# Kernel tuning notes

Hardware: AMD Instinct MI355X
Metric: run time of the kernel (lower is better)

## Reference

```python
import jax, jax.numpy as jnp
import numpy as np

N_NODES = 50000
N_EDGES = 400000
N_GRAPHS = 16
IN_DIM_NODE = 6
IN_DIM_EDGE = 2
HIDDEN = 64
N_LAYERS = 3
STATE_DIM = 4
MLP1, MLP2 = 256, 256
MAX_ACTION = 1.0
BN_EPS = 1e-5


def _lin(key, fan_in, fan_out):
    k1, k2 = jax.random.split(key)
    s = 1.0 / np.sqrt(fan_in)
    w = jax.random.uniform(k1, (fan_in, fan_out), minval=-s, maxval=s, dtype=jnp.float32)
    b = jax.random.uniform(k2, (fan_out,), minval=-s, maxval=s, dtype=jnp.float32)
    return w, b


def setup_inputs() -> dict:
    key = jax.random.key(0)
    ks = jax.random.split(key, 32)
    inp = {}
    inp["state"] = jax.random.normal(ks[0], (N_GRAPHS, STATE_DIM), dtype=jnp.float32)
    inp["h_feat"] = jax.random.normal(ks[1], (N_NODES, IN_DIM_NODE), dtype=jnp.float32)
    # positive edge features (distances) bounded away from 0 since forward takes 1/e
    inp["e_feat"] = jax.random.uniform(ks[2], (N_EDGES, IN_DIM_EDGE), minval=0.5, maxval=1.5, dtype=jnp.float32)
    inp["src"] = jax.random.randint(ks[3], (N_EDGES,), 0, N_NODES, dtype=jnp.int32)
    inp["dst"] = jax.random.randint(ks[4], (N_EDGES,), 0, N_NODES, dtype=jnp.int32)
    inp["graph_ids"] = jnp.sort(jax.random.randint(ks[5], (N_NODES,), 0, N_GRAPHS, dtype=jnp.int32))
    inp["emb_h_w"], inp["emb_h_b"] = _lin(ks[6], IN_DIM_NODE, HIDDEN)
    inp["emb_e_w"], inp["emb_e_b"] = _lin(ks[7], IN_DIM_EDGE, HIDDEN)
    for i, name in enumerate(["A", "B", "C", "D", "E"]):
        ws, bs = [], []
        for l in range(N_LAYERS):
            w, b = _lin(jax.random.fold_in(ks[8 + i], l), HIDDEN, HIDDEN)
            ws.append(w); bs.append(b)
        inp[name + "_w"] = jnp.stack(ws)  # [L, H, H]
        inp[name + "_b"] = jnp.stack(bs)  # [L, H]
    inp["bn_h_g"] = jnp.ones((N_LAYERS, HIDDEN), jnp.float32)
    inp["bn_h_b"] = jnp.zeros((N_LAYERS, HIDDEN), jnp.float32)
    inp["bn_e_g"] = jnp.ones((N_LAYERS, HIDDEN), jnp.float32)
    inp["bn_e_b"] = jnp.zeros((N_LAYERS, HIDDEN), jnp.float32)
    inp["l1_w"], inp["l1_b"] = _lin(ks[13], HIDDEN + STATE_DIM, MLP1)
    inp["l2_w"], inp["l2_b"] = _lin(ks[14], MLP1, MLP2)
    inp["l3_w"], inp["l3_b"] = _lin(ks[15], MLP2, 2)
    return inp


def _bn(x, g, b):
    mu = jnp.mean(x, axis=0)
    var = jnp.var(x, axis=0)
    return (x - mu) * jax.lax.rsqrt(var + BN_EPS) * g + b


def reference(state, h_feat, e_feat, src, dst, graph_ids,
              emb_h_w, emb_h_b, emb_e_w, emb_e_b,
              A_w, A_b, B_w, B_b, C_w, C_b, D_w, D_b, E_w, E_b,
              bn_h_g, bn_h_b, bn_e_g, bn_e_b,
              l1_w, l1_b, l2_w, l2_b, l3_w, l3_b):
    N = h_feat.shape[0]
    B = state.shape[0]
    # feature prep: concat node states, reciprocal edge states
    e = 1.0 / e_feat
    h = h_feat @ emb_h_w + emb_h_b          # [N, H]
    e = e @ emb_e_w + emb_e_b               # [E, H]
    for l in range(N_LAYERS):
        h_in, e_in = h, e
        Ah = h @ A_w[l] + A_b[l]
        Bh = h @ B_w[l] + B_b[l]
        Dh = h @ D_w[l] + D_b[l]
        Eh = h @ E_w[l] + E_b[l]
        Ce = e @ C_w[l] + C_b[l]
        e_hat = Dh[src] + Eh[dst] + Ce      # [E, H] edge gates pre-activation
        sigma = jax.nn.sigmoid(e_hat)
        num = jax.ops.segment_sum(sigma * Bh[src], dst, num_segments=N)
        den = jax.ops.segment_sum(sigma, dst, num_segments=N)
        h_new = Ah + num / (den + 1e-6)
        h = h_in + jax.nn.relu(_bn(h_new, bn_h_g[l], bn_h_b[l]))
        e = e_in + jax.nn.relu(_bn(e_hat, bn_e_g[l], bn_e_b[l]))
    # mean readout per graph
    counts = jax.ops.segment_sum(jnp.ones((N,), h.dtype), graph_ids, num_segments=B)
    hg = jax.ops.segment_sum(h, graph_ids, num_segments=B) / counts[:, None]
    x = jnp.concatenate([hg, state], axis=-1)
    x = jax.nn.relu(x @ l1_w + l1_b)
    x = jax.nn.relu(x @ l2_w + l2_b)
    return MAX_ACTION * jnp.tanh(x @ l3_w + l3_b)
```

## Files before the change

kernel.cpp:

```cpp
#include <hip/hip_runtime.h>
#include <hip/hip_fp16.h>
#include <math.h>
#include <string.h>

#define NN 50000
#define NE 400000

__device__ __forceinline__ void atomAddF(float* p, float v) { unsafeAtomicAdd(p, v); }
__device__ __forceinline__ double atomAddD(double* p, double v) { return unsafeAtomicAdd(p, v); }
__device__ __forceinline__ int atomAddI(int* p, int v) { return atomicAdd(p, v); }

typedef _Float16 h2v __attribute__((ext_vector_type(2)));

__device__ __forceinline__ float2 up2h(unsigned v) {
  __half2 h; memcpy(&h, &v, 4); return __half22float2(h);
}
__device__ __forceinline__ unsigned pk2h(float a, float b) {
  __half2 h = __floats2half2_rn(a, b);
  unsigned v; memcpy(&v, &h, 4); return v;
}
__device__ __forceinline__ void up8(uint4 u, float* f) {
  float2 a = up2h(u.x), b = up2h(u.y), c = up2h(u.z), d = up2h(u.w);
  f[0] = a.x; f[1] = a.y; f[2] = b.x; f[3] = b.y;
  f[4] = c.x; f[5] = c.y; f[6] = d.x; f[7] = d.y;
}
__device__ __forceinline__ uint4 pk8(const float* f) {
  uint4 u;
  u.x = pk2h(f[0], f[1]); u.y = pk2h(f[2], f[3]);
  u.z = pk2h(f[4], f[5]); u.w = pk2h(f[6], f[7]);
  return u;
}

#if __has_builtin(__builtin_amdgcn_fdot2)
__device__ __forceinline__ float dot2(unsigned a, unsigned b, float c) {
  return __builtin_amdgcn_fdot2(__builtin_bit_cast(h2v, a), __builtin_bit_cast(h2v, b), c, false);
}
#else
__device__ __forceinline__ float dot2(unsigned a, unsigned b, float c) {
  float2 fa = up2h(a), fb = up2h(b);
  return c + fa.x * fb.x + fa.y * fb.y;
}
#endif

#define SW(kk) ((((kk) & 7)) << 2)

__global__ __launch_bounds__(256) void k_zero(float4* __restrict__ p, int n4) {
  int i = blockIdx.x * 256 + threadIdx.x;
  int s = gridDim.x * 256;
  for (; i < n4; i += s) p[i] = make_float4(0.f, 0.f, 0.f, 0.f);
}

__global__ __launch_bounds__(256) void k_deg(const int* __restrict__ dst, int* __restrict__ deg) {
  int i = blockIdx.x * 256 + threadIdx.x;
  if (i < NE) atomAddI(&deg[dst[i]], 1);
}

__global__ __launch_bounds__(1024) void k_scan(int* __restrict__ degcur,
    int* __restrict__ offs, double* __restrict__ stats) {
  __shared__ int wsum[16];
  int t = threadIdx.x;
  int lane = t & 63, w = t >> 6;
  if (t < 256) stats[t] = 0.0;
  int carry = 0;
  for (int base = 0; base < NN; base += 1024) {
    int i = base + t;
    int v = (i < NN) ? degcur[i] : 0;
    int x = v;
    #pragma unroll
    for (int off = 1; off < 64; off <<= 1) {
      int y = __shfl_up(x, off);
      if (lane >= off) x += y;
    }
    if (lane == 63) wsum[w] = x;
    __syncthreads();
    if (w == 0 && lane < 16) {
      int s = wsum[lane];
      #pragma unroll
      for (int off = 1; off < 16; off <<= 1) {
        int y = __shfl_up(s, off);
        if (lane >= off) s += y;
      }
      wsum[lane] = s;
    }
    __syncthreads();
    int wbase = (w > 0) ? wsum[w - 1] : 0;
    int total = wsum[15];
    int excl = carry + wbase + x - v;
    if (i < NN) { offs[i] = excl; degcur[i] = excl; }
    carry += total;
    __syncthreads();
  }
  if (t == 0) offs[NN] = carry;
}

__global__ __launch_bounds__(256) void k_scatter(const int* __restrict__ dst,
    const int* __restrict__ src, const float* __restrict__ e_feat,
    int* __restrict__ cursor,
    int* __restrict__ srcp, int* __restrict__ dstp, float* __restrict__ ef2) {
  int i = blockIdx.x * 256 + threadIdx.x;
  if (i < NE) {
    int d = dst[i];
    int p = atomAddI(&cursor[d], 1);
    srcp[p] = src[i];
    dstp[p] = d;
    ((float2*)ef2)[p] = ((const float2*)e_feat)[i];
  }
}

template <int MODE>
__global__ __launch_bounds__(512) void k_node_gemm(float* __restrict__ h,
    const float* __restrict__ Ah_in, const float* __restrict__ bnp,
    const float* __restrict__ hf, const float* __restrict__ ehw,
    const float* __restrict__ ehb,
    const float* __restrict__ w0, const float* __restrict__ w1,
    const float* __restrict__ w2, const float* __restrict__ w3,
    const float* __restrict__ b0, const float* __restrict__ b1,
    const float* __restrict__ b2, const float* __restrict__ b3,
    float* __restrict__ Ah, __half* __restrict__ Bh16,
    __half* __restrict__ Dh16, __half* __restrict__ Eh16) {
  __shared__ __align__(16) unsigned hsU[32 * 256];
  __shared__ __align__(16) unsigned wshU[32 * 64];
  int t = threadIdx.x;
  int n0 = blockIdx.x * 256;
  #pragma unroll
  for (int i = 0; i < 8; ++i) {
    int f = (t + i * 512) * 4;
    int r = f >> 6;
    int k = f & 63;
    int n = n0 + r;
    float4 v = make_float4(0.f, 0.f, 0.f, 0.f);
    if (n < NN) {
      size_t idx = (size_t)n * 64 + k;
      if (MODE == 2) {
        const float* row = hf + (size_t)n * 6;
        v = *(const float4*)(ehb + k);
        #pragma unroll
        for (int q = 0; q < 6; ++q) {
          float x = row[q];
          float4 wv = *(const float4*)(ehw + q * 64 + k);
          v.x += x * wv.x; v.y += x * wv.y; v.z += x * wv.z; v.w += x * wv.w;
        }
        *(float4*)(h + idx) = v;
      } else {
        v = *(const float4*)(h + idx);
        if (MODE == 1) {
          float4 av = *(const float4*)(Ah_in + idx);
          float4 sc4 = *(const float4*)(bnp + k);
          float4 sh4 = *(const float4*)(bnp + 64 + k);
          v.x += fmaxf(av.x * sc4.x + sh4.x, 0.f);
          v.y += fmaxf(av.y * sc4.y + sh4.y, 0.f);
          v.z += fmaxf(av.z * sc4.z + sh4.z, 0.f);
          v.w += fmaxf(av.w * sc4.w + sh4.w, 0.f);
          *(float4*)(h + idx) = v;
        }
      }
    }
    int kk0 = k >> 1;
    hsU[(kk0 + 0) * 256 + (r ^ SW(kk0 + 0))] = pk2h(v.x, v.y);
    hsU[(kk0 + 1) * 256 + (r ^ SW(kk0 + 1))] = pk2h(v.z, v.w);
  }
  int cg = t & 7, rg = t >> 3;
  int cb = cg * 8;
  #pragma unroll 1
  for (int y = 0; y < 4; ++y) {
    const float* W = (y == 0) ? w0 : (y == 1) ? w1 : (y == 2) ? w2 : w3;
    const float* B = (y == 0) ? b0 : (y == 1) ? b1 : (y == 2) ? b2 : b3;
    __syncthreads();
    #pragma unroll
    for (int i = 0; i < 4; ++i) {
      int idx = t + i * 512;
      int kk = idx >> 6, j = idx & 63;
      wshU[idx] = pk2h(W[(2 * kk) * 64 + j], W[(2 * kk + 1) * 64 + j]);
    }
    __syncthreads();
    float acc[4][8];
    #pragma unroll
    for (int r = 0; r < 4; ++r)
      #pragma unroll
      for (int j = 0; j < 8; ++j) acc[r][j] = 0.f;
    #pragma unroll 8
    for (int kk = 0; kk < 32; ++kk) {
      uint4 a4 = *(const uint4*)&hsU[kk * 256 + ((rg * 4) ^ SW(kk))];
      uint4 wA = *(const uint4*)&wshU[kk * 64 + cb];
      uint4 wB = *(const uint4*)&wshU[kk * 64 + cb + 4];
      unsigned av[4] = {a4.x, a4.y, a4.z, a4.w};
      unsigned wv[8] = {wA.x, wA.y, wA.z, wA.w, wB.x, wB.y, wB.z, wB.w};
      #pragma unroll
      for (int r = 0; r < 4; ++r)
        #pragma unroll
        for (int j = 0; j < 8; ++j) acc[r][j] = dot2(av[r], wv[j], acc[r][j]);
    }
    float4 bv0 = *(const float4*)(B + cb);
    float4 bv1 = *(const float4*)(B + cb + 4);
    float bv[8] = {bv0.x, bv0.y, bv0.z, bv0.w, bv1.x, bv1.y, bv1.z, bv1.w};
    __half* oh = (y == 1) ? Bh16 : (y == 2) ? Dh16 : Eh16;
    #pragma unroll
    for (int r = 0; r < 4; ++r) {
      int n = n0 + rg * 4 + r;
      if (n < NN) {
        float o[8];
        #pragma unroll
        for (int j = 0; j < 8; ++j) o[j] = acc[r][j] + bv[j];
        if (y == 0) {
          *(float4*)(Ah + (size_t)n * 64 + cb) = make_float4(o[0], o[1], o[2], o[3]);
          *(float4*)(Ah + (size_t)n * 64 + cb + 4) = make_float4(o[4], o[5], o[6], o[7]);
        } else {
          *(uint4*)(oh + (size_t)n * 64 + cb) = pk8(o);
        }
      }
    }
  }
}

template <int MODE, int ESTATS, int EWRITE>
__global__ __launch_bounds__(512) void k_edge_f(__half* __restrict__ e16,
    __half* __restrict__ eh16,
    const float* __restrict__ Cw, const float* __restrict__ Cb,
    const int* __restrict__ srcp, const int* __restrict__ dstp,
    const __half* __restrict__ Dh16, const __half* __restrict__ Eh16,
    const float* __restrict__ bnp, double* __restrict__ stats,
    const float* __restrict__ ef2, const float* __restrict__ ew,
    const float* __restrict__ eb) {
  __shared__ __align__(16) unsigned esU[32 * 256];
  __shared__ __align__(16) unsigned cwU[32 * 64];
  int t = threadIdx.x;
  int e0 = blockIdx.x * 256;
  #pragma unroll
  for (int i = 0; i < 4; ++i) {
    int idx = t + i * 512;
    int kk = idx >> 6, j = idx & 63;
    cwU[idx] = pk2h(Cw[(2 * kk) * 64 + j], Cw[(2 * kk + 1) * 64 + j]);
  }
  #pragma unroll
  for (int i = 0; i < 4; ++i) {
    int f = (t + i * 512) * 8;
    int r = f >> 6;
    int k = f & 63;
    int row = e0 + r;
    uint4 raw = make_uint4(0u, 0u, 0u, 0u);
    if (row < NE) {
      size_t idx = (size_t)row * 64 + k;
      if (MODE == 2) {
        float2 rp = ((const float2*)ef2)[row];
        float r0 = 1.0f / rp.x;
        float r1 = 1.0f / rp.y;
        float4 bA = *(const float4*)(eb + k), bB = *(const float4*)(eb + k + 4);
        float4 waA = *(const float4*)(ew + k), waB = *(const float4*)(ew + k + 4);
        float4 wbA = *(const float4*)(ew + 64 + k), wbB = *(const float4*)(ew + 64 + k + 4);
        float v[8];
        v[0] = bA.x + r0 * waA.x + r1 * wbA.x;
        v[1] = bA.y + r0 * waA.y + r1 * wbA.y;
        v[2] = bA.z + r0 * waA.z + r1 * wbA.z;
        v[3] = bA.w + r0 * waA.w + r1 * wbA.w;
        v[4] = bB.x + r0 * waB.x + r1 * wbB.x;
        v[5] = bB.y + r0 * waB.y + r1 * wbB.y;
        v[6] = bB.z + r0 * waB.z + r1 * wbB.z;
        v[7] = bB.w + r0 * waB.w + r1 * wbB.w;
        raw = pk8(v);
        if (EWRITE) *(uint4*)(e16 + idx) = raw;
      } else {
        raw = *(const uint4*)(e16 + idx);
        if (MODE == 1) {
          float v[8], pp[8];
          up8(raw, v);
          up8(*(const uint4*)(eh16 + idx), pp);
          float4 scA = *(const float4*)(bnp + 128 + k);
          float4 scB = *(const float4*)(bnp + 128 + k + 4);
          float4 shA = *(const float4*)(bnp + 192 + k);
          float4 shB = *(const float4*)(bnp + 192 + k + 4);
          float sc[8] = {scA.x, scA.y, scA.z, scA.w, scB.x, scB.y, scB.z, scB.w};
          float sh[8] = {shA.x, shA.y, shA.z, shA.w, shB.x, shB.y, shB.z, shB.w};
          #pragma unroll
          for (int j = 0; j < 8; ++j) v[j] += fmaxf(pp[j] * sc[j] + sh[j], 0.f);
          raw = pk8(v);
          if (EWRITE) *(uint4*)(e16 + idx) = raw;
        }
      }
    }
    int kk0 = k >> 1;
    esU[(kk0 + 0) * 256 + (r ^ SW(kk0 + 0))] = raw.x;
    esU[(kk0 + 1) * 256 + (r ^ SW(kk0 + 1))] = raw.y;
    esU[(kk0 + 2) * 256 + (r ^ SW(kk0 + 2))] = raw.z;
    esU[(kk0 + 3) * 256 + (r ^ SW(kk0 + 3))] = raw.w;
  }
  __syncthreads();
  int cg = t & 7, rg = t >> 3;
  int cb = cg * 8;
  float acc[4][8];
  #pragma unroll
  for (int r = 0; r < 4; ++r)
    #pragma unroll
    for (int j = 0; j < 8; ++j) acc[r][j] = 0.f;
  #pragma unroll 8
  for (int kk = 0; kk < 32; ++kk) {
    uint4 a4 = *(const uint4*)&esU[kk * 256 + ((rg * 4) ^ SW(kk))];
    uint4 wA = *(const uint4*)&cwU[kk * 64 + cb];
    uint4 wB = *(const uint4*)&cwU[kk * 64 + cb + 4];
    unsigned av[4] = {a4.x, a4.y, a4.z, a4.w};
    unsigned wv[8] = {wA.x, wA.y, wA.z, wA.w, wB.x, wB.y, wB.z, wB.w};
    #pragma unroll
    for (int r = 0; r < 4; ++r)
      #pragma unroll
      for (int j = 0; j < 8; ++j) acc[r][j] = dot2(av[r], wv[j], acc[r][j]);
  }
  float4 cb0 = *(const float4*)(Cb + cb);
  float4 cb1 = *(const float4*)(Cb + cb + 4);
  float cbv[8] = {cb0.x, cb0.y, cb0.z, cb0.w, cb1.x, cb1.y, cb1.z, cb1.w};
  float psum[8], psq[8];
  #pragma unroll
  for (int j = 0; j < 8; ++j) { psum[j] = 0.f; psq[j] = 0.f; }
  #pragma unroll
  for (int r = 0; r < 4; ++r) {
    int p = e0 + rg * 4 + r;
    if (p < NE) {
      int sN = srcp[p], dN = dstp[p];
      float dd[8], qq[8];
      up8(*(const uint4*)(Dh16 + (size_t)sN * 64 + cb), dd);
      up8(*(const uint4*)(Eh16 + (size_t)dN * 64 + cb), qq);
      float ev[8];
      #pragma unroll
      for (int j = 0; j < 8; ++j) {
        float v = acc[r][j] + cbv[j] + dd[j] + qq[j];
        ev[j] = v;
        if (ESTATS) { psum[j] += v; psq[j] += v * v; }
      }
      *(uint4*)(eh16 + (size_t)p * 64 + cb) = pk8(ev);
    }
  }
  if (ESTATS) {
    float* red = (float*)esU;
    __syncthreads();
    #pragma unroll
    for (int j = 0; j < 8; ++j) red[rg * 65 + cb + j] = psum[j];
    __syncthreads();
    if (t < 64) {
      float s = 0.f;
      #pragma unroll
      for (int i = 0; i < 64; ++i) s += red[i * 65 + t];
      atomAddD(stats + 128 + t, (double)s);
    }
    __syncthreads();
    #pragma unroll
    for (int j = 0; j < 8; ++j) red[rg * 65 + cb + j] = psq[j];
    __syncthreads();
    if (t < 64) {
      float q = 0.f;
      #pragma unroll
      for (int i = 0; i < 64; ++i) q += red[i * 65 + t];
      atomAddD(stats + 192 + t, (double)q);
    }
  }
}

template <int LAST>
__global__ __launch_bounds__(1024) void k_agg(const int* __restrict__ offs,
    const int* __restrict__ srcp, const __half* __restrict__ eh16,
    const __half* __restrict__ Bh16, float* __restrict__ Ah, double* __restrict__ stats,
    int* __restrict__ ctr,
    const float* __restrict__ hgam, const float* __restrict__ hbet,
    const float* __restrict__ egam, const float* __restrict__ ebet,
    float* __restrict__ bnp, float* __restrict__ hg) {
  int t = threadIdx.x;
  int c = t & 63;
  int g = t >> 6;
  float psum = 0.f, psq = 0.f;
  #pragma unroll 1
  for (int sub = 0; sub < 8; ++sub) {
    int n = blockIdx.x * 128 + g * 8 + sub;
    if (n < NN) {
      int i0 = offs[n], i1 = offs[n + 1];
      float num = 0.f, den = 0.f;
      int i = i0;
      #pragma unroll 1
      for (; i + 3 < i1; i += 4) {
        float x0 = __half2float(eh16[(size_t)(i + 0) * 64 + c]);
        float x1 = __half2float(eh16[(size_t)(i + 1) * 64 + c]);
        float x2 = __half2float(eh16[(size_t)(i + 2) * 64 + c]);
        float x3 = __half2float(eh16[(size_t)(i + 3) * 64 + c]);
        int s0 = srcp[i], s1 = srcp[i + 1], s2 = srcp[i + 2], s3 = srcp[i + 3];
        float b0 = __half2float(Bh16[(size_t)s0 * 64 + c]);
        float b1 = __half2float(Bh16[(size_t)s1 * 64 + c]);
        float b2 = __half2float(Bh16[(size_t)s2 * 64 + c]);
        float b3 = __half2float(Bh16[(size_t)s3 * 64 + c]);
        float g0 = 1.0f / (1.0f + __expf(-x0));
        float g1 = 1.0f / (1.0f + __expf(-x1));
        float g2 = 1.0f / (1.0f + __expf(-x2));
        float g3 = 1.0f / (1.0f + __expf(-x3));
        num += g0 * b0 + g1 * b1 + g2 * b2 + g3 * b3;
        den += g0 + g1 + g2 + g3;
      }
      #pragma unroll 1
      for (; i < i1; ++i) {
        float x0 = __half2float(eh16[(size_t)i * 64 + c]);
        int s0 = srcp[i];
        float b0 = __half2float(Bh16[(size_t)s0 * 64 + c]);
        float g0 = 1.0f / (1.0f + __expf(-x0));
        num += g0 * b0;
        den += g0;
      }
      float v = Ah[(size_t)n * 64 + c] + num / (den + 1e-6f);
      Ah[(size_t)n * 64 + c] = v;
      psum += v; psq += v * v;
    }
  }
  __shared__ float red[1024];
  red[t] = psum; __syncthreads();
  if (t < 64) {
    float s = 0.f;
    #pragma unroll
    for (int i = 0; i < 16; ++i) s += red[t + i * 64];
    atomAddD(stats + t, (double)s);
  }
  __syncthreads();
  red[t] = psq; __syncthreads();
  if (t < 64) {
    float q = 0.f;
    #pragma unroll
    for (int i = 0; i < 16; ++i) q += red[t + i * 64];
    atomAddD(stats + 64 + t, (double)q);
  }
  __shared__ int lastFlag;
  __syncthreads();
  if (t == 0) {
    __threadfence();
    int old = atomAddI(ctr, 1);
    lastFlag = (old == (int)gridDim.x - 1);
  }
  __syncthreads();
  if (!lastFlag) return;
  if (t < 64) {
    double s = atomAddD(stats + t, 0.0);
    double q = atomAddD(stats + 64 + t, 0.0);
    double mu = s * (1.0 / NN);
    double var = q * (1.0 / NN) - mu * mu;
    float sc = hgam[t] / sqrtf((float)var + 1e-5f);
    bnp[t] = sc;
    bnp[64 + t] = hbet[t] - (float)mu * sc;
  } else if (t < 128) {
    int cc = t - 64;
    double s = atomAddD(stats + 128 + cc, 0.0);
    double q = atomAddD(stats + 192 + cc, 0.0);
    double mu = s * (1.0 / NE);
    double var = q * (1.0 / NE) - mu * mu;
    float sc = egam[cc] / sqrtf((float)var + 1e-5f);
    bnp[128 + cc] = sc;
    bnp[192 + cc] = ebet[cc] - (float)mu * sc;
  }
  __syncthreads();
  if (t < 256) atomicExch((unsigned long long*)&stats[t], 0ull);
  if (LAST) {
    for (int i = t; i < 1040; i += 1024) hg[i] = 0.f;
  }
}

__global__ __launch_bounds__(256) void k_readout(const float* __restrict__ h,
    const float* __restrict__ Ah, const float* __restrict__ bnp,
    const int* __restrict__ gid, float* __restrict__ hg, float* __restrict__ counts) {
  int t = threadIdx.x;
  int c = t & 63;
  int ro = t >> 6;
  int nbase = blockIdx.x * 256;
  float sc = bnp[c], sh = bnp[64 + c];
  float sum = 0.f, cnt = 0.f;
  int curg = -1;
  #pragma unroll 1
  for (int i = 0; i < 64; ++i) {
    int n = nbase + ro + i * 4;
    if (n >= NN) break;
    int g = gid[n];
    if (g != curg) {
      if (curg >= 0) {
        atomAddF(&hg[curg * 64 + c], sum);
        if (c == 0) atomAddF(&counts[curg], cnt);
      }
      curg = g; sum = 0.f; cnt = 0.f;
    }
    size_t idx = (size_t)n * 64 + c;
    sum += h[idx] + fmaxf(Ah[idx] * sc + sh, 0.f);
    cnt += 1.f;
  }
  if (curg >= 0) {
    atomAddF(&hg[curg * 64 + c], sum);
    if (c == 0) atomAddF(&counts[curg], cnt);
  }
}

__global__ __launch_bounds__(256) void k_mlp(const float* __restrict__ hg, const float* __restrict__ counts,
    const float* __restrict__ state,
    const float* __restrict__ w1, const float* __restrict__ b1,
    const float* __restrict__ w2, const float* __restrict__ b2,
    const float* __restrict__ w3, const float* __restrict__ b3,
    float* __restrict__ out) {
  __shared__ float x0[16][68];
  __shared__ float x1[16][256];
  __shared__ float x2[16][256];
  int t = threadIdx.x;
  for (int idx = t; idx < 16 * 68; idx += 256) {
    int g = idx / 68, c = idx % 68;
    x0[g][c] = (c < 64) ? hg[g * 64 + c] / counts[g] : state[g * 4 + (c - 64)];
  }
  __syncthreads();
  {
    float acc[16];
    float bb = b1[t];
    #pragma unroll
    for (int g = 0; g < 16; ++g) acc[g] = bb;
    for (int k = 0; k < 68; ++k) {
      float w = w1[k * 256 + t];
      #pragma unroll
      for (int g = 0; g < 16; ++g) acc[g] += x0[g][k] * w;
    }
    #pragma unroll
    for (int g = 0; g < 16; ++g) x1[g][t] = fmaxf(acc[g], 0.f);
  }
  __syncthreads();
  {
    float acc[16];
    float bb = b2[t];
    #pragma unroll
    for (int g = 0; g < 16; ++g) acc[g] = bb;
    for (int k = 0; k < 256; ++k) {
      float w = w2[k * 256 + t];
      #pragma unroll
      for (int g = 0; g < 16; ++g) acc[g] += x1[g][k] * w;
    }
    #pragma unroll
    for (int g = 0; g < 16; ++g) x2[g][t] = fmaxf(acc[g], 0.f);
  }
  __syncthreads();
  if (t < 32) {
    int g = t >> 1, o = t & 1;
    float acc = b3[o];
    for (int k = 0; k < 256; ++k) acc += x2[g][k] * w3[k * 2 + o];
    out[g * 2 + o] = tanhf(acc);
  }
}

extern "C" void kernel_launch(void* const* d_in, const int* in_sizes, int n_in,
                              void* d_out, int out_size, void* d_ws, size_t ws_size,
                              hipStream_t stream) {
  const float* state   = (const float*)d_in[0];
  const float* h_feat  = (const float*)d_in[1];
  const float* e_feat  = (const float*)d_in[2];
  const int*   src     = (const int*)d_in[3];
  const int*   dst     = (const int*)d_in[4];
  const int*   gid     = (const int*)d_in[5];
  const float* emb_h_w = (const float*)d_in[6];
  const float* emb_h_b = (const float*)d_in[7];
  const float* emb_e_w = (const float*)d_in[8];
  const float* emb_e_b = (const float*)d_in[9];
  const float* A_w = (const float*)d_in[10];
  const float* A_b = (const float*)d_in[11];
  const float* B_w = (const float*)d_in[12];
  const float* B_b = (const float*)d_in[13];
  const float* C_w = (const float*)d_in[14];
  const float* C_b = (const float*)d_in[15];
  const float* D_w = (const float*)d_in[16];
  const float* D_b = (const float*)d_in[17];
  const float* E_w = (const float*)d_in[18];
  const float* E_b = (const float*)d_in[19];
  const float* bn_h_g = (const float*)d_in[20];
  const float* bn_h_b = (const float*)d_in[21];
  const float* bn_e_g = (const float*)d_in[22];
  const float* bn_e_b = (const float*)d_in[23];
  const float* l1_w = (const float*)d_in[24];
  const float* l1_b = (const float*)d_in[25];
  const float* l2_w = (const float*)d_in[26];
  const float* l2_b = (const float*)d_in[27];
  const float* l3_w = (const float*)d_in[28];
  const float* l3_b = (const float*)d_in[29];

  float* wsp = (float*)d_ws;

  const size_t F_H = (size_t)NN * 64;
  const size_t F_H2 = (size_t)NN * 32;
  const size_t F_E2 = (size_t)NE * 32;
  size_t off = 0;
  float*  h     = wsp + off; off += F_H;
  float*  Ah    = wsp + off; off += F_H;
  __half* e16   = (__half*)(wsp + off); off += F_E2;
  __half* eh16  = (__half*)(wsp + off); off += F_E2;
  float*  ef2   = wsp + off; off += (size_t)NE * 2;
  __half* Bh16  = (__half*)(wsp + off); off += F_H2;
  __half* Dh16  = (__half*)(wsp + off); off += F_H2;
  __half* Eh16  = (__half*)(wsp + off); off += F_H2;
  int* srcp    = (int*)(wsp + off); off += NE;
  int* dstp    = (int*)(wsp + off); off += NE;
  int* offs    = (int*)(wsp + off); off += NN + 4;
  int* degcur  = (int*)(wsp + off); off += NN + 4;
  double* stats = (double*)(wsp + off); off += 512;
  float* bnp    = wsp + off; off += 256;
  float* hg     = wsp + off; off += 1024;
  float* counts = hg + 1024; off += 16;
  const size_t need = off * sizeof(float);
  if (ws_size < need) return;
  int* ctr = degcur + NN;

  k_zero<<<64, 256, 0, stream>>>((float4*)degcur, (NN + 4) / 4);
  k_deg<<<(NE + 255) / 256, 256, 0, stream>>>(dst, degcur);
  k_scan<<<1, 1024, 0, stream>>>(degcur, offs, stats);
  k_scatter<<<(NE + 255) / 256, 256, 0, stream>>>(dst, src, e_feat, degcur, srcp, dstp, ef2);

  const int GN = (NN + 255) / 256;
  const int GE = (NE + 255) / 256;
  const int GA = (NN + 127) / 128;
  for (int l = 0; l < 3; ++l) {
    if (l == 0)
      k_node_gemm<2><<<GN, 512, 0, stream>>>(h, Ah, bnp, h_feat, emb_h_w, emb_h_b,
          A_w, B_w, D_w, E_w, A_b, B_b, D_b, E_b, Ah, Bh16, Dh16, Eh16);
    else
      k_node_gemm<1><<<GN, 512, 0, stream>>>(h, Ah, bnp, h_feat, emb_h_w, emb_h_b,
          A_w + l * 4096, B_w + l * 4096, D_w + l * 4096, E_w + l * 4096,
          A_b + l * 64, B_b + l * 64, D_b + l * 64, E_b + l * 64,
          Ah, Bh16, Dh16, Eh16);
    if (l == 0)
      k_edge_f<2, 1, 1><<<GE, 512, 0, stream>>>(e16, eh16, C_w, C_b,
          srcp, dstp, Dh16, Eh16, bnp, stats, ef2, emb_e_w, emb_e_b);
    else if (l == 1)
      k_edge_f<1, 1, 1><<<GE, 512, 0, stream>>>(e16, eh16, C_w + 4096, C_b + 64,
          srcp, dstp, Dh16, Eh16, bnp, stats, ef2, emb_e_w, emb_e_b);
    else
      k_edge_f<1, 0, 0><<<GE, 512, 0, stream>>>(e16, eh16, C_w + 8192, C_b + 128,
          srcp, dstp, Dh16, Eh16, bnp, stats, ef2, emb_e_w, emb_e_b);
    if (l < 2)
      k_agg<0><<<GA, 1024, 0, stream>>>(offs, srcp, eh16, Bh16, Ah, stats, ctr + l,
          bn_h_g + l * 64, bn_h_b + l * 64, bn_e_g + l * 64, bn_e_b + l * 64, bnp, hg);
    else
      k_agg<1><<<GA, 1024, 0, stream>>>(offs, srcp, eh16, Bh16, Ah, stats, ctr + l,
          bn_h_g + l * 64, bn_h_b + l * 64, bn_e_g + l * 64, bn_e_b + l * 64, bnp, hg);
  }
  k_readout<<<(NN + 255) / 256, 256, 0, stream>>>(h, Ah, bnp, gid, hg, counts);
  k_mlp<<<1, 256, 0, stream>>>(hg, counts, state,
      l1_w, l1_b, l2_w, l2_b, l3_w, l3_b, (float*)d_out);
}
```

Measured before the change: 591.6 us.

## Store Ah in fp16 and vectorize aggregation to two channels per thread

Result: no change. 601.6 us (+1.7%).

```diff
diff --git a/kernel.cpp b/kernel.cpp
--- a/kernel.cpp
+++ b/kernel.cpp
@@ -109,14 +109,14 @@
 
 template <int MODE>
 __global__ __launch_bounds__(512) void k_node_gemm(float* __restrict__ h,
-    const float* __restrict__ Ah_in, const float* __restrict__ bnp,
+    const __half* __restrict__ Ah_in, const float* __restrict__ bnp,
     const float* __restrict__ hf, const float* __restrict__ ehw,
     const float* __restrict__ ehb,
     const float* __restrict__ w0, const float* __restrict__ w1,
     const float* __restrict__ w2, const float* __restrict__ w3,
     const float* __restrict__ b0, const float* __restrict__ b1,
     const float* __restrict__ b2, const float* __restrict__ b3,
-    float* __restrict__ Ah, __half* __restrict__ Bh16,
+    __half* __restrict__ Ah16, __half* __restrict__ Bh16,
     __half* __restrict__ Dh16, __half* __restrict__ Eh16) {
   __shared__ __align__(16) unsigned hsU[32 * 256];
   __shared__ __align__(16) unsigned wshU[32 * 64];
@@ -144,13 +144,14 @@
       } else {
         v = *(const float4*)(h + idx);
         if (MODE == 1) {
-          float4 av = *(const float4*)(Ah_in + idx);
+          uint2 au = *(const uint2*)(Ah_in + idx);
+          float2 a01 = up2h(au.x), a23 = up2h(au.y);
           float4 sc4 = *(const float4*)(bnp + k);
           float4 sh4 = *(const float4*)(bnp + 64 + k);
-          v.x += fmaxf(av.x * sc4.x + sh4.x, 0.f);
-          v.y += fmaxf(av.y * sc4.y + sh4.y, 0.f);
-          v.z += fmaxf(av.z * sc4.z + sh4.z, 0.f);
-          v.w += fmaxf(av.w * sc4.w + sh4.w, 0.f);
+          v.x += fmaxf(a01.x * sc4.x + sh4.x, 0.f);
+          v.y += fmaxf(a01.y * sc4.y + sh4.y, 0.f);
+          v.z += fmaxf(a23.x * sc4.z + sh4.z, 0.f);
+          v.w += fmaxf(a23.y * sc4.w + sh4.w, 0.f);
           *(float4*)(h + idx) = v;
         }
       }
@@ -193,7 +194,7 @@
     float4 bv0 = *(const float4*)(B + cb);
     float4 bv1 = *(const float4*)(B + cb + 4);
     float bv[8] = {bv0.x, bv0.y, bv0.z, bv0.w, bv1.x, bv1.y, bv1.z, bv1.w};
-    __half* oh = (y == 1) ? Bh16 : (y == 2) ? Dh16 : Eh16;
+    __half* oh = (y == 0) ? Ah16 : (y == 1) ? Bh16 : (y == 2) ? Dh16 : Eh16;
     #pragma unroll
     for (int r = 0; r < 4; ++r) {
       int n = n0 + rg * 4 + r;
@@ -201,12 +202,7 @@
         float o[8];
         #pragma unroll
         for (int j = 0; j < 8; ++j) o[j] = acc[r][j] + bv[j];
-        if (y == 0) {
-          *(float4*)(Ah + (size_t)n * 64 + cb) = make_float4(o[0], o[1], o[2], o[3]);
-          *(float4*)(Ah + (size_t)n * 64 + cb + 4) = make_float4(o[4], o[5], o[6], o[7]);
-        } else {
-          *(uint4*)(oh + (size_t)n * 64 + cb) = pk8(o);
-        }
+        *(uint4*)(oh + (size_t)n * 64 + cb) = pk8(o);
       }
     }
   }
@@ -355,68 +351,85 @@
 template <int LAST>
 __global__ __launch_bounds__(1024) void k_agg(const int* __restrict__ offs,
     const int* __restrict__ srcp, const __half* __restrict__ eh16,
-    const __half* __restrict__ Bh16, float* __restrict__ Ah, double* __restrict__ stats,
+    const __half* __restrict__ Bh16, __half* __restrict__ Ah16, double* __restrict__ stats,
     int* __restrict__ ctr,
     const float* __restrict__ hgam, const float* __restrict__ hbet,
     const float* __restrict__ egam, const float* __restrict__ ebet,
     float* __restrict__ bnp, float* __restrict__ hg) {
   int t = threadIdx.x;
-  int c = t & 63;
-  int g = t >> 6;
-  float psum = 0.f, psq = 0.f;
+  int c2 = (t & 31) * 2;
+  int g = t >> 5;
+  float psx = 0.f, psy = 0.f, pqx = 0.f, pqy = 0.f;
   #pragma unroll 1
-  for (int sub = 0; sub < 8; ++sub) {
-    int n = blockIdx.x * 128 + g * 8 + sub;
+  for (int sub = 0; sub < 4; ++sub) {
+    int n = blockIdx.x * 128 + g * 4 + sub;
     if (n < NN) {
       int i0 = offs[n], i1 = offs[n + 1];
-      float num = 0.f, den = 0.f;
+      float nx = 0.f, ny = 0.f, dx = 0.f, dy = 0.f;
       int i = i0;
       #pragma unroll 1
       for (; i + 3 < i1; i += 4) {
-        float x0 = __half2float(eh16[(size_t)(i + 0) * 64 + c]);
-        float x1 = __half2float(eh16[(size_t)(i + 1) * 64 + c]);
-        float x2 = __half2float(eh16[(size_t)(i + 2) * 64 + c]);
-        float x3 = __half2float(eh16[(size_t)(i + 3) * 64 + c]);
+        unsigned xu0 = *(const unsigned*)(eh16 + (size_t)(i + 0) * 64 + c2);
+        unsigned xu1 = *(const unsigned*)(eh16 + (size_t)(i + 1) * 64 + c2);
+        unsigned xu2 = *(const unsigned*)(eh16 + (size_t)(i + 2) * 64 + c2);
+        unsigned xu3 = *(const unsigned*)(eh16 + (size_t)(i + 3) * 64 + c2);
         int s0 = srcp[i], s1 = srcp[i + 1], s2 = srcp[i + 2], s3 = srcp[i + 3];
-        float b0 = __half2float(Bh16[(size_t)s0 * 64 + c]);
-        float b1 = __half2float(Bh16[(size_t)s1 * 64 + c]);
-        float b2 = __half2float(Bh16[(size_t)s2 * 64 + c]);
-        float b3 = __half2float(Bh16[(size_t)s3 * 64 + c]);
-        float g0 = 1.0f / (1.0f + __expf(-x0));
-        float g1 = 1.0f / (1.0f + __expf(-x1));
-        float g2 = 1.0f / (1.0f + __expf(-x2));
-        float g3 = 1.0f / (1.0f + __expf(-x3));
-        num += g0 * b0 + g1 * b1 + g2 * b2 + g3 * b3;
-        den += g0 + g1 + g2 + g3;
+        unsigned bu0 = *(const unsigned*)(Bh16 + (size_t)s0 * 64 + c2);
+        unsigned bu1 = *(const unsigned*)(Bh16 + (size_t)s1 * 64 + c2);
+        unsigned bu2 = *(const unsigned*)(Bh16 + (size_t)s2 * 64 + c2);
+        unsigned bu3 = *(const unsigned*)(Bh16 + (size_t)s3 * 64 + c2);
+        float2 x0 = up2h(xu0), x1 = up2h(xu1), x2 = up2h(xu2), x3 = up2h(xu3);
+        float2 b0 = up2h(bu0), b1 = up2h(bu1), b2 = up2h(bu2), b3 = up2h(bu3);
+        float g0x = 1.0f / (1.0f + __expf(-x0.x)), g0y = 1.0f / (1.0f + __expf(-x0.y));
+        float g1x = 1.0f / (1.0f + __expf(-x1.x)), g1y = 1.0f / (1.0f + __expf(-x1.y));
+        float g2x = 1.0f / (1.0f + __expf(-x2.x)), g2y = 1.0f / (1.0f + __expf(-x2.y));
+        float g3x = 1.0f / (1.0f + __expf(-x3.x)), g3y = 1.0f / (1.0f + __expf(-x3.y));
+        nx += g0x * b0.x + g1x * b1.x + g2x * b2.x + g3x * b3.x;
+        ny += g0y * b0.y + g1y * b1.y + g2y * b2.y + g3y * b3.y;
+        dx += g0x + g1x + g2x + g3x;
+        dy += g0y + g1y + g2y + g3y;
       }
       #pragma unroll 1
       for (; i < i1; ++i) {
-        float x0 = __half2float(eh16[(size_t)i * 64 + c]);
+        unsigned xu = *(const unsigned*)(eh16 + (size_t)i * 64 + c2);
         int s0 = srcp[i];
-        float b0 = __half2float(Bh16[(size_t)s0 * 64 + c]);
-        float g0 = 1.0f / (1.0f + __expf(-x0));
-        num += g0 * b0;
-        den += g0;
-      }
-      float v = Ah[(size_t)n * 64 + c] + num / (den + 1e-6f);
-      Ah[(size_t)n * 64 + c] = v;
-      psum += v; psq += v * v;
-    }
-  }
-  __shared__ float red[1024];
-  red[t] = psum; __syncthreads();
+        unsigned bu = *(const unsigned*)(Bh16 + (size_t)s0 * 64 + c2);
+        float2 x = up2h(xu), b = up2h(bu);
+        float gx = 1.0f / (1.0f + __expf(-x.x)), gy = 1.0f / (1.0f + __expf(-x.y));
+        nx += gx * b.x; ny += gy * b.y;
+        dx += gx; dy += gy;
+      }
+      size_t idx = (size_t)n * 64 + c2;
+      float2 a = up2h(*(const unsigned*)(Ah16 + idx));
+      float vx = a.x + nx / (dx + 1e-6f);
+      float vy = a.y + ny / (dy + 1e-6f);
+      *(unsigned*)(Ah16 + idx) = pk2h(vx, vy);
+      psx += vx; psy += vy;
+      pqx += vx * vx; pqy += vy * vy;
+    }
+  }
+  __shared__ float2 red2[1024];
+  red2[t] = make_float2(psx, psy); __syncthreads();
   if (t < 64) {
+    int p = t >> 1, j = t & 1;
     float s = 0.f;
     #pragma unroll
-    for (int i = 0; i < 16; ++i) s += red[t + i * 64];
+    for (int i = 0; i < 32; ++i) {
+      float2 v = red2[i * 32 + p];
+      s += j ? v.y : v.x;
+    }
     atomAddD(stats + t, (double)s);
   }
   __syncthreads();
-  red[t] = psq; __syncthreads();
+  red2[t] = make_float2(pqx, pqy); __syncthreads();
   if (t < 64) {
+    int p = t >> 1, j = t & 1;
     float q = 0.f;
     #pragma unroll
-    for (int i = 0; i < 16; ++i) q += red[t + i * 64];
+    for (int i = 0; i < 32; ++i) {
+      float2 v = red2[i * 32 + p];
+      q += j ? v.y : v.x;
+    }
     atomAddD(stats + 64 + t, (double)q);
   }
   __shared__ int lastFlag;
@@ -454,7 +467,7 @@
 }
 
 __global__ __launch_bounds__(256) void k_readout(const float* __restrict__ h,
-    const float* __restrict__ Ah, const float* __restrict__ bnp,
+    const __half* __restrict__ Ah16, const float* __restrict__ bnp,
     const int* __restrict__ gid, float* __restrict__ hg, float* __restrict__ counts) {
   int t = threadIdx.x;
   int c = t & 63;
@@ -476,7 +489,8 @@
       curg = g; sum = 0.f; cnt = 0.f;
     }
     size_t idx = (size_t)n * 64 + c;
-    sum += h[idx] + fmaxf(Ah[idx] * sc + sh, 0.f);
+    float av = __half2float(Ah16[idx]);
+    sum += h[idx] + fmaxf(av * sc + sh, 0.f);
     cnt += 1.f;
   }
   if (curg >= 0) {
@@ -577,7 +591,7 @@
   const size_t F_E2 = (size_t)NE * 32;
   size_t off = 0;
   float*  h     = wsp + off; off += F_H;
-  float*  Ah    = wsp + off; off += F_H;
+  __half* Ah16  = (__half*)(wsp + off); off += F_H2;
   __half* e16   = (__half*)(wsp + off); off += F_E2;
   __half* eh16  = (__half*)(wsp + off); off += F_E2;
   float*  ef2   = wsp + off; off += (size_t)NE * 2;
@@ -606,13 +620,13 @@
   const int GA = (NN + 127) / 128;
   for (int l = 0; l < 3; ++l) {
     if (l == 0)
-      k_node_gemm<2><<<GN, 512, 0, stream>>>(h, Ah, bnp, h_feat, emb_h_w, emb_h_b,
-          A_w, B_w, D_w, E_w, A_b, B_b, D_b, E_b, Ah, Bh16, Dh16, Eh16);
+      k_node_gemm<2><<<GN, 512, 0, stream>>>(h, Ah16, bnp, h_feat, emb_h_w, emb_h_b,
+          A_w, B_w, D_w, E_w, A_b, B_b, D_b, E_b, Ah16, Bh16, Dh16, Eh16);
     else
-      k_node_gemm<1><<<GN, 512, 0, stream>>>(h, Ah, bnp, h_feat, emb_h_w, emb_h_b,
+      k_node_gemm<1><<<GN, 512, 0, stream>>>(h, Ah16, bnp, h_feat, emb_h_w, emb_h_b,
           A_w + l * 4096, B_w + l * 4096, D_w + l * 4096, E_w + l * 4096,
           A_b + l * 64, B_b + l * 64, D_b + l * 64, E_b + l * 64,
-          Ah, Bh16, Dh16, Eh16);
+          Ah16, Bh16, Dh16, Eh16);
     if (l == 0)
       k_edge_f<2, 1, 1><<<GE, 512, 0, stream>>>(e16, eh16, C_w, C_b,
           srcp, dstp, Dh16, Eh16, bnp, stats, ef2, emb_e_w, emb_e_b);
@@ -623,13 +637,13 @@
       k_edge_f<1, 0, 0><<<GE, 512, 0, stream>>>(e16, eh16, C_w + 8192, C_b + 128,
           srcp, dstp, Dh16, Eh16, bnp, stats, ef2, emb_e_w, emb_e_b);
     if (l < 2)
-      k_agg<0><<<GA, 1024, 0, stream>>>(offs, srcp, eh16, Bh16, Ah, stats, ctr + l,
+      k_agg<0><<<GA, 1024, 0, stream>>>(offs, srcp, eh16, Bh16, Ah16, stats, ctr + l,
           bn_h_g + l * 64, bn_h_b + l * 64, bn_e_g + l * 64, bn_e_b + l * 64, bnp, hg);
     else
-      k_agg<1><<<GA, 1024, 0, stream>>>(offs, srcp, eh16, Bh16, Ah, stats, ctr + l,
+      k_agg<1><<<GA, 1024, 0, stream>>>(offs, srcp, eh16, Bh16, Ah16, stats, ctr + l,
           bn_h_g + l * 64, bn_h_b + l * 64, bn_e_g + l * 64, bn_e_b + l * 64, bnp, hg);
   }
-  k_readout<<<(NN + 255) / 256, 256, 0, stream>>>(h, Ah, bnp, gid, hg, counts);
+  k_readout<<<(NN + 255) / 256, 256, 0, stream>>>(h, Ah16, bnp, gid, hg, counts);
   k_mlp<<<1, 256, 0, stream>>>(hg, counts, state,
       l1_w, l1_b, l2_w, l2_b, l3_w, l3_b, (float*)d_out);
 }
```
